# Performance work log

Hardware: AMD Instinct MI355X
Metric: run time of the kernel (lower is better)

Reference implementation:

```python
import jax, jax.numpy as jnp
import numpy as np
import math

B, S, H, D = 4, 4096, 2048, 128  # batch, seq_len, hidden_dim, head_size

def setup_inputs() -> dict:
    key = jax.random.key(0)
    ks = jax.random.split(key, 7)
    scale = 1.0 / math.sqrt(H)
    return {
        "x": jax.random.normal(ks[0], (B, S, H), dtype=jnp.float32),
        "Wq": jax.random.normal(ks[1], (H, D), dtype=jnp.float32) * scale,
        "bq": jnp.zeros((D,), dtype=jnp.float32),
        "Wk": jax.random.normal(ks[2], (H, D), dtype=jnp.float32) * scale,
        "bk": jnp.zeros((D,), dtype=jnp.float32),
        "Wv": jax.random.normal(ks[3], (H, D), dtype=jnp.float32) * scale,
        "bv": jnp.zeros((D,), dtype=jnp.float32),
    }

def reference(x, Wq, bq, Wk, bk, Wv, bv):
    # projections: [B,S,D]
    q = x @ Wq + bq
    k = x @ Wk + bk
    v = x @ Wv + bv
    # raw scores [B,S,S] with causal mask, NO pre-softmax scaling (as in source)
    scores = jnp.einsum('bsd,btd->bst', q, k)
    causal = jnp.tril(jnp.ones((S, S), dtype=bool))
    scores = jnp.where(causal, scores, -jnp.inf)
    # non-standard: scale AFTER softmax by 1/sqrt(head_size)
    w = jax.nn.softmax(scores, axis=-1) * (1.0 / math.sqrt(D))
    # dropout p=0.0 -> identity
    return jnp.einsum('bst,btd->bsd', w, v)
```

## Files before the change

kernel.cpp:

```cpp
#include <hip/hip_runtime.h>
#include <math.h>
#include <stdint.h>

#define SEQ   4096
#define HID   2048
#define HD    128
#define NROWS 16384

typedef __attribute__((ext_vector_type(8))) short bf16x8;
typedef __attribute__((ext_vector_type(4))) float f32x4;

static constexpr float OSCALE = 0.088388347648318447f;

using gvptr = const __attribute__((address_space(1))) void*;
using lvptr = __attribute__((address_space(3))) void*;
__device__ __forceinline__ void gld_lds16(const void* g, void* l) {
    __builtin_amdgcn_global_load_lds((gvptr)g, (lvptr)l, 16, 0, 0);
}

__device__ __forceinline__ unsigned short f2bf_rne(float f) {
    union { float f; unsigned u; } v; v.f = f;
    unsigned u = v.u + 0x7fffu + ((v.u >> 16) & 1u);
    return (unsigned short)(u >> 16);
}
__device__ __forceinline__ unsigned short f2bf_tr(float f) {
    union { float f; unsigned u; } v; v.f = f;
    return (unsigned short)(v.u >> 16);
}
__device__ __forceinline__ float bf2f(unsigned short h) {
    union { unsigned u; float f; } v; v.u = ((unsigned)h) << 16;
    return v.f;
}

__global__ __launch_bounds__(256) void prep_w(
    const float* __restrict__ Wq, const float* __restrict__ Wk, const float* __restrict__ Wv,
    unsigned short* __restrict__ wth, unsigned short* __restrict__ wtl)
{
    __shared__ float T[64][68];
    const int tid = threadIdx.x;
    const int k0 = blockIdx.x * 64, n0 = blockIdx.y * 64, mm = blockIdx.z;
    const float* W = (mm == 0) ? Wq : (mm == 1) ? Wk : Wv;
    #pragma unroll
    for (int i = 0; i < 4; ++i) {
        const int fi = i * 256 + tid, kk = fi >> 4, nc = (fi & 15) * 4;
        const float4 w = *(const float4*)(W + (size_t)(k0 + kk) * HD + n0 + nc);
        T[kk][nc] = w.x; T[kk][nc + 1] = w.y; T[kk][nc + 2] = w.z; T[kk][nc + 3] = w.w;
    }
    __syncthreads();
    unsigned short* oh = wth + (size_t)mm * HD * HID;
    unsigned short* ol = wtl + (size_t)mm * HD * HID;
    #pragma unroll
    for (int i = 0; i < 4; ++i) {
        const int fi = i * 256 + tid, nn = fi >> 4, kc = (fi & 15) * 4;
        const float a = T[kc][nn], b = T[kc + 1][nn], c = T[kc + 2][nn], d = T[kc + 3][nn];
        ushort4 hv, lv;
        hv.x = f2bf_rne(a); hv.y = f2bf_rne(b); hv.z = f2bf_rne(c); hv.w = f2bf_rne(d);
        lv.x = f2bf_rne(a - bf2f(hv.x)); lv.y = f2bf_rne(b - bf2f(hv.y));
        lv.z = f2bf_rne(c - bf2f(hv.z)); lv.w = f2bf_rne(d - bf2f(hv.w));
        *(ushort4*)(oh + (size_t)(n0 + nn) * HID + k0 + kc) = hv;
        *(ushort4*)(ol + (size_t)(n0 + nn) * HID + k0 + kc) = lv;
    }
}

__global__ __launch_bounds__(256, 3) void qkv_split(
    const float* __restrict__ x,
    const float* __restrict__ bq, const float* __restrict__ bk, const float* __restrict__ bv,
    const unsigned short* __restrict__ wth, const unsigned short* __restrict__ wtl,
    unsigned short* __restrict__ qh, unsigned short* __restrict__ ql,
    unsigned short* __restrict__ kh, unsigned short* __restrict__ kl,
    unsigned short* __restrict__ vth)
{
    __shared__ unsigned short Ah[64][64], Al[64][64];
    __shared__ unsigned short Bh[128][64], Bl[128][64];

    const int tid = threadIdx.x, wave = tid >> 6, lane = tid & 63;
    const int l15 = lane & 15, q4 = lane >> 4;
    const int wr = wave >> 1, wc = wave & 1;
    const int type = blockIdx.x % 3;
    const int tile = blockIdx.x / 3;
    const int r0 = tile * 64;
    const bool qk = (type < 2);

    const unsigned short* wh = wth + (size_t)type * HD * HID;
    const unsigned short* wl = wtl + (size_t)type * HD * HID;

    const int srow   = lane >> 3;
    const int schunk = ((lane & 7) ^ srow) * 8;

    f32x4 acc[2][4];
    #pragma unroll
    for (int mt = 0; mt < 2; ++mt)
        #pragma unroll
        for (int nt = 0; nt < 4; ++nt)
            acc[mt][nt] = (f32x4){0.f, 0.f, 0.f, 0.f};

    const float* xbase = x + (size_t)r0 * HID;

    float4 xv[4];
    #pragma unroll
    for (int i = 0; i < 4; ++i) {
        const int fi = i * 256 + tid, row = fi >> 4, kc = (fi & 15) * 4;
        xv[i] = *(const float4*)(xbase + (size_t)row * HID + kc);
    }

    for (int k0 = 0; k0 < HID; k0 += 64) {
        __syncthreads();

        {
            #pragma unroll
            for (int c = 0; c < 4; ++c) {
                const int row = wave * 32 + c * 8;
                gld_lds16(wh + (size_t)(row + srow) * HID + k0 + schunk, &Bh[row][0]);
            }
            if (qk) {
                #pragma unroll
                for (int c = 0; c < 4; ++c) {
                    const int row = wave * 32 + c * 8;
                    gld_lds16(wl + (size_t)(row + srow) * HID + k0 + schunk, &Bl[row][0]);
                }
            }
        }
        #pragma unroll
        for (int i = 0; i < 4; ++i) {
            const int fi = i * 256 + tid, row = fi >> 4, kc = (fi & 15) * 4;
            const int pk = ((kc >> 3) ^ (row & 7)) * 8 + (kc & 7);
            ushort4 hv;
            hv.x = f2bf_tr(xv[i].x); hv.y = f2bf_tr(xv[i].y);
            hv.z = f2bf_tr(xv[i].z); hv.w = f2bf_tr(xv[i].w);
            *(ushort4*)&Ah[row][pk] = hv;
            if (qk) {
                ushort4 lv;
                lv.x = f2bf_tr(xv[i].x - bf2f(hv.x)); lv.y = f2bf_tr(xv[i].y - bf2f(hv.y));
                lv.z = f2bf_tr(xv[i].z - bf2f(hv.z)); lv.w = f2bf_tr(xv[i].w - bf2f(hv.w));
                *(ushort4*)&Al[row][pk] = lv;
            }
        }
        __syncthreads();

        const int kn = (k0 + 64 < HID) ? (k0 + 64) : 0;
        #pragma unroll
        for (int i = 0; i < 4; ++i) {
            const int fi = i * 256 + tid, row = fi >> 4, kc = (fi & 15) * 4;
            xv[i] = *(const float4*)(xbase + (size_t)row * HID + kn + kc);
        }

        #pragma unroll
        for (int ks = 0; ks < 2; ++ks) {
            const int pc = ((ks * 4 + q4) ^ (l15 & 7)) * 8;
            bf16x8 ah[2], al[2];
            #pragma unroll
            for (int mt = 0; mt < 2; ++mt) {
                const int ar = wr * 32 + mt * 16 + l15;
                ah[mt] = *(const bf16x8*)&Ah[ar][pc];
                if (qk) al[mt] = *(const bf16x8*)&Al[ar][pc];
            }
            #pragma unroll
            for (int nt = 0; nt < 4; ++nt) {
                const int br = wc * 64 + nt * 16 + l15;
                const bf16x8 bh = *(const bf16x8*)&Bh[br][pc];
                #pragma unroll
                for (int mt = 0; mt < 2; ++mt)
                    acc[mt][nt] = __builtin_amdgcn_mfma_f32_16x16x32_bf16(ah[mt], bh, acc[mt][nt], 0, 0, 0);
                if (qk) {
                    const bf16x8 bl = *(const bf16x8*)&Bl[br][pc];
                    #pragma unroll
                    for (int mt = 0; mt < 2; ++mt) {
                        acc[mt][nt] = __builtin_amdgcn_mfma_f32_16x16x32_bf16(ah[mt], bl, acc[mt][nt], 0, 0, 0);
                        acc[mt][nt] = __builtin_amdgcn_mfma_f32_16x16x32_bf16(al[mt], bh, acc[mt][nt], 0, 0, 0);
                    }
                }
            }
        }
    }

    if (qk) {
        const float* bb = (type == 0) ? bq : bk;
        unsigned short* oh = (type == 0) ? qh : kh;
        unsigned short* ol = (type == 0) ? ql : kl;
        #pragma unroll
        for (int nt = 0; nt < 4; ++nt) {
            const int col = wc * 64 + nt * 16 + l15;
            const float bias = bb[col];
            #pragma unroll
            for (int mt = 0; mt < 2; ++mt) {
                const int Rb = r0 + wr * 32 + mt * 16 + q4 * 4;
                #pragma unroll
                for (int r = 0; r < 4; ++r) {
                    const float v = acc[mt][nt][r] + bias;
                    const unsigned short h = f2bf_rne(v);
                    oh[(size_t)(Rb + r) * HD + col] = h;
                    ol[(size_t)(Rb + r) * HD + col] = f2bf_rne(v - bf2f(h));
                }
            }
        }
    } else {
        #pragma unroll
        for (int nt = 0; nt < 4; ++nt) {
            const int col = wc * 64 + nt * 16 + l15;
            const float bias = bv[col];
            #pragma unroll
            for (int mt = 0; mt < 2; ++mt) {
                const int Rb = r0 + wr * 32 + mt * 16 + q4 * 4;
                const int bi = Rb >> 12, s0 = Rb & 4095;
                ushort4 pv;
                pv.x = f2bf_rne(acc[mt][nt][0] + bias);
                pv.y = f2bf_rne(acc[mt][nt][1] + bias);
                pv.z = f2bf_rne(acc[mt][nt][2] + bias);
                pv.w = f2bf_rne(acc[mt][nt][3] + bias);
                *(ushort4*)(vth + ((size_t)(bi * HD + col)) * SEQ + s0) = pv;
            }
        }
    }
}

__global__ __launch_bounds__(256, 2) void flash_mfma(
    const unsigned short* __restrict__ qh, const unsigned short* __restrict__ ql,
    const unsigned short* __restrict__ kh, const unsigned short* __restrict__ kl,
    const unsigned short* __restrict__ vth,
    unsigned short* __restrict__ oPb, float* __restrict__ mP, float* __restrict__ lP)
{
    __shared__ unsigned short Kh[64][128], Kl[64][128];
    __shared__ unsigned short Vt[128][64];
    __shared__ unsigned short Ps[4][16][72];

    const int tid = threadIdx.x, wave = tid >> 6, lane = tid & 63;
    const int l15 = lane & 15, q4 = lane >> 4;
    const int h = blockIdx.x & 3, pair = (blockIdx.x >> 2) & 31, b = blockIdx.x >> 7;

    const int krow_l = lane >> 4;
    const int vrow_l = lane >> 3;
    const int vsc = ((lane & 7) ^ (vrow_l & 7)) * 8;
    const int kkey7 = l15 & 7;
    const int vkey7 = l15 & 7;

    for (int side = 0; side < 2; ++side) {
        const int tt = side ? (63 - pair) : pair;
        const int n = tt + 1;
        const int j0 = (n * h) >> 2, j1 = (n * (h + 1)) >> 2;

        const int qrow = b * SEQ + tt * 64 + wave * 16 + l15;
        bf16x8 aqh[4], aql[4];
        #pragma unroll
        for (int ks = 0; ks < 4; ++ks) {
            aqh[ks] = *(const bf16x8*)(qh + (size_t)qrow * HD + ks * 32 + q4 * 8);
            aql[ks] = *(const bf16x8*)(ql + (size_t)qrow * HD + ks * 32 + q4 * 8);
        }
        f32x4 oa[8];
        #pragma unroll
        for (int d = 0; d < 8; ++d) oa[d] = (f32x4){0.f, 0.f, 0.f, 0.f};
        float m_r[4] = {-INFINITY, -INFINITY, -INFINITY, -INFINITY};
        float l_r[4] = {0.f, 0.f, 0.f, 0.f};

        for (int j = j0; j < j1; ++j) {
            __syncthreads();
            {
                const size_t kb = (size_t)b * SEQ + j * 64;
                #pragma unroll
                for (int c = 0; c < 4; ++c) {
                    const int rl = c * 4 + krow_l;
                    const int sc = (l15 ^ (rl & 7)) * 8;
                    const size_t gr = (kb + wave * 16 + rl) * HD + sc;
                    gld_lds16(kh + gr, &Kh[wave * 16 + c * 4][0]);
                    gld_lds16(kl + gr, &Kl[wave * 16 + c * 4][0]);
                }
                #pragma unroll
                for (int c = 0; c < 4; ++c)
                    gld_lds16(vth + ((size_t)(b * HD + wave * 32 + c * 8 + vrow_l)) * SEQ
                                  + j * 64 + vsc,
                              &Vt[wave * 32 + c * 8][0]);
            }
            __syncthreads();

            f32x4 s[4];
            #pragma unroll
            for (int nt = 0; nt < 4; ++nt) s[nt] = (f32x4){0.f, 0.f, 0.f, 0.f};
            #pragma unroll
            for (int ks = 0; ks < 4; ++ks) {
                const int pc = ((ks * 4 + q4) ^ kkey7) * 8;
                #pragma unroll
                for (int nt = 0; nt < 4; ++nt) {
                    const bf16x8 bh = *(const bf16x8*)&Kh[nt * 16 + l15][pc];
                    const bf16x8 bl = *(const bf16x8*)&Kl[nt * 16 + l15][pc];
                    s[nt] = __builtin_amdgcn_mfma_f32_16x16x32_bf16(aqh[ks], bh, s[nt], 0, 0, 0);
                    s[nt] = __builtin_amdgcn_mfma_f32_16x16x32_bf16(aql[ks], bh, s[nt], 0, 0, 0);
                    s[nt] = __builtin_amdgcn_mfma_f32_16x16x32_bf16(aqh[ks], bl, s[nt], 0, 0, 0);
                }
            }
            if (j == tt) {
                #pragma unroll
                for (int nt = 0; nt < 4; ++nt) {
                    const int cl = nt * 16 + l15;
                    #pragma unroll
                    for (int r = 0; r < 4; ++r) {
                        const int rl = wave * 16 + q4 * 4 + r;
                        if (cl > rl) s[nt][r] = -INFINITY;
                    }
                }
            }
            #pragma unroll
            for (int r = 0; r < 4; ++r) {
                float mt = fmaxf(fmaxf(s[0][r], s[1][r]), fmaxf(s[2][r], s[3][r]));
                mt = fmaxf(mt, __shfl_xor(mt, 1));
                mt = fmaxf(mt, __shfl_xor(mt, 2));
                mt = fmaxf(mt, __shfl_xor(mt, 4));
                mt = fmaxf(mt, __shfl_xor(mt, 8));
                const float mn = fmaxf(m_r[r], mt);
                const float al = __expf(m_r[r] - mn);
                m_r[r] = mn;
                const float p0 = __expf(s[0][r] - mn), p1 = __expf(s[1][r] - mn);
                const float p2 = __expf(s[2][r] - mn), p3 = __expf(s[3][r] - mn);
                Ps[wave][q4 * 4 + r][l15]      = f2bf_tr(p0);
                Ps[wave][q4 * 4 + r][16 + l15] = f2bf_tr(p1);
                Ps[wave][q4 * 4 + r][32 + l15] = f2bf_tr(p2);
                Ps[wave][q4 * 4 + r][48 + l15] = f2bf_tr(p3);
                float ps = p0 + p1 + p2 + p3;
                ps += __shfl_xor(ps, 1); ps += __shfl_xor(ps, 2);
                ps += __shfl_xor(ps, 4); ps += __shfl_xor(ps, 8);
                l_r[r] = l_r[r] * al + ps;
                #pragma unroll
                for (int d = 0; d < 8; ++d) oa[d][r] *= al;
            }
            const bf16x8 ap0 = *(const bf16x8*)&Ps[wave][l15][q4 * 8];
            const bf16x8 ap1 = *(const bf16x8*)&Ps[wave][l15][32 + q4 * 8];
            #pragma unroll
            for (int d = 0; d < 8; ++d) {
                const bf16x8 bv0 = *(const bf16x8*)&Vt[d * 16 + l15][(q4 ^ vkey7) * 8];
                const bf16x8 bv1 = *(const bf16x8*)&Vt[d * 16 + l15][((4 + q4) ^ vkey7) * 8];
                oa[d] = __builtin_amdgcn_mfma_f32_16x16x32_bf16(ap0, bv0, oa[d], 0, 0, 0);
                oa[d] = __builtin_amdgcn_mfma_f32_16x16x32_bf16(ap1, bv1, oa[d], 0, 0, 0);
            }
        }

        const int R0 = b * SEQ + tt * 64 + wave * 16 + q4 * 4;
        unsigned short* op = oPb + (size_t)h * NROWS * HD;
        #pragma unroll
        for (int d = 0; d < 8; ++d)
            #pragma unroll
            for (int r = 0; r < 4; ++r)
                op[(size_t)(R0 + r) * HD + d * 16 + l15] = f2bf_rne(oa[d][r]);
        if (l15 == 0) {
            #pragma unroll
            for (int r = 0; r < 4; ++r) {
                mP[h * NROWS + R0 + r] = m_r[r];
                lP[h * NROWS + R0 + r] = l_r[r];
            }
        }
    }
}

__global__ __launch_bounds__(256) void flash_merge(
    const unsigned short* __restrict__ oPb, const float* __restrict__ mP,
    const float* __restrict__ lP, float* __restrict__ out)
{
    const int idx = blockIdx.x * 256 + threadIdx.x;
    const int r = idx >> 5, c = (idx & 31) * 4;
    float m[4], l[4];
    #pragma unroll
    for (int i = 0; i < 4; ++i) { m[i] = mP[i * NROWS + r]; l[i] = lP[i * NROWS + r]; }
    float M = fmaxf(fmaxf(m[0], m[1]), fmaxf(m[2], m[3]));
    float a[4], lsum = 0.f;
    #pragma unroll
    for (int i = 0; i < 4; ++i) { a[i] = __expf(m[i] - M); lsum += l[i] * a[i]; }
    const float inv = OSCALE / lsum;
    float ox = 0.f, oy = 0.f, oz = 0.f, ow = 0.f;
    #pragma unroll
    for (int i = 0; i < 4; ++i) {
        const ushort4 ov = *(const ushort4*)(oPb + (size_t)i * NROWS * HD + (size_t)r * HD + c);
        ox += a[i] * bf2f(ov.x); oy += a[i] * bf2f(ov.y);
        oz += a[i] * bf2f(ov.z); ow += a[i] * bf2f(ov.w);
    }
    float4 o; o.x = ox * inv; o.y = oy * inv; o.z = oz * inv; o.w = ow * inv;
    *(float4*)(out + (size_t)r * HD + c) = o;
}

extern "C" void kernel_launch(void* const* d_in, const int* in_sizes, int n_in,
                              void* d_out, int out_size, void* d_ws, size_t ws_size,
                              hipStream_t stream)
{
    (void)in_sizes; (void)n_in; (void)out_size; (void)ws_size;
    const float* x  = (const float*)d_in[0];
    const float* Wq = (const float*)d_in[1];
    const float* bq = (const float*)d_in[2];
    const float* Wk = (const float*)d_in[3];
    const float* bk = (const float*)d_in[4];
    const float* Wv = (const float*)d_in[5];
    const float* bv = (const float*)d_in[6];
    float* out = (float*)d_out;

    char* w = (char*)d_ws;
    unsigned short* qh  = (unsigned short*)(w);
    unsigned short* ql  = (unsigned short*)(w + 4194304);
    unsigned short* kh  = (unsigned short*)(w + 8388608);
    unsigned short* kl  = (unsigned short*)(w + 12582912);
    unsigned short* vth = (unsigned short*)(w + 16777216);
    unsigned short* wth = (unsigned short*)(w + 20971520);
    unsigned short* wtl = (unsigned short*)(w + 22544384);
    unsigned short* oPb = (unsigned short*)(w + 24117248);
    float* mP = (float*)(w + 40894464);
    float* lP = (float*)(w + 41156608);

    prep_w<<<dim3(32, 2, 3), 256, 0, stream>>>(Wq, Wk, Wv, wth, wtl);
    qkv_split<<<768, 256, 0, stream>>>(x, bq, bk, bv, wth, wtl, qh, ql, kh, kl, vth);
    flash_mfma<<<512, 256, 0, stream>>>(qh, ql, kh, kl, vth, oPb, mP, lP);
    flash_merge<<<2048, 256, 0, stream>>>(oPb, mP, lP, out);
}
```

Measured before the change: 311.4 us.

## Transpose QK^T MFMA layout, add lazy max rescale and MFMA priority hints

Swaps the MFMA operands for the score tile so each lane holds one query row's scores across its register slots. Row max and sum reductions then need only two cross-lane shuffles instead of four per row. The P tile is written to LDS as packed 4-wide stores. A wave-wide lazy rescale skips the exp correction and output rescale whenever no row's max grows by more than 8, and s_setprio is raised around the MFMA blocks. The lazy threshold lets unnormalized exponentials reach e^8, which is safe in fp32 but adds a per-tile vote and a branch.

Result: faster. 304.0 us (-2.4%).

```diff
diff --git a/kernel.cpp b/kernel.cpp
--- a/kernel.cpp
+++ b/kernel.cpp
@@ -248,8 +248,8 @@
         f32x4 oa[8];
         #pragma unroll
         for (int d = 0; d < 8; ++d) oa[d] = (f32x4){0.f, 0.f, 0.f, 0.f};
-        float m_r[4] = {-INFINITY, -INFINITY, -INFINITY, -INFINITY};
-        float l_r[4] = {0.f, 0.f, 0.f, 0.f};
+        float m_r = -INFINITY;
+        float l_r = 0.f;
 
         for (int j = j0; j < j1; ++j) {
             __syncthreads();
@@ -274,6 +274,7 @@
             f32x4 s[4];
             #pragma unroll
             for (int nt = 0; nt < 4; ++nt) s[nt] = (f32x4){0.f, 0.f, 0.f, 0.f};
+            __builtin_amdgcn_s_setprio(1);
             #pragma unroll
             for (int ks = 0; ks < 4; ++ks) {
                 const int pc = ((ks * 4 + q4) ^ kkey7) * 8;
@@ -281,47 +282,73 @@
                 for (int nt = 0; nt < 4; ++nt) {
                     const bf16x8 bh = *(const bf16x8*)&Kh[nt * 16 + l15][pc];
                     const bf16x8 bl = *(const bf16x8*)&Kl[nt * 16 + l15][pc];
-                    s[nt] = __builtin_amdgcn_mfma_f32_16x16x32_bf16(aqh[ks], bh, s[nt], 0, 0, 0);
-                    s[nt] = __builtin_amdgcn_mfma_f32_16x16x32_bf16(aql[ks], bh, s[nt], 0, 0, 0);
-                    s[nt] = __builtin_amdgcn_mfma_f32_16x16x32_bf16(aqh[ks], bl, s[nt], 0, 0, 0);
-                }
-            }
+                    s[nt] = __builtin_amdgcn_mfma_f32_16x16x32_bf16(bh, aqh[ks], s[nt], 0, 0, 0);
+                    s[nt] = __builtin_amdgcn_mfma_f32_16x16x32_bf16(bh, aql[ks], s[nt], 0, 0, 0);
+                    s[nt] = __builtin_amdgcn_mfma_f32_16x16x32_bf16(bl, aqh[ks], s[nt], 0, 0, 0);
+                }
+            }
+            __builtin_amdgcn_s_setprio(0);
+
             if (j == tt) {
-                #pragma unroll
-                for (int nt = 0; nt < 4; ++nt) {
-                    const int cl = nt * 16 + l15;
+                const int qloc = wave * 16 + l15;
+                #pragma unroll
+                for (int nt = 0; nt < 4; ++nt)
                     #pragma unroll
                     for (int r = 0; r < 4; ++r) {
-                        const int rl = wave * 16 + q4 * 4 + r;
-                        if (cl > rl) s[nt][r] = -INFINITY;
+                        const int kvl = nt * 16 + q4 * 4 + r;
+                        if (kvl > qloc) s[nt][r] = -INFINITY;
                     }
-                }
-            }
-            #pragma unroll
-            for (int r = 0; r < 4; ++r) {
-                float mt = fmaxf(fmaxf(s[0][r], s[1][r]), fmaxf(s[2][r], s[3][r]));
-                mt = fmaxf(mt, __shfl_xor(mt, 1));
-                mt = fmaxf(mt, __shfl_xor(mt, 2));
-                mt = fmaxf(mt, __shfl_xor(mt, 4));
-                mt = fmaxf(mt, __shfl_xor(mt, 8));
-                const float mn = fmaxf(m_r[r], mt);
-                const float al = __expf(m_r[r] - mn);
-                m_r[r] = mn;
-                const float p0 = __expf(s[0][r] - mn), p1 = __expf(s[1][r] - mn);
-                const float p2 = __expf(s[2][r] - mn), p3 = __expf(s[3][r] - mn);
-                Ps[wave][q4 * 4 + r][l15]      = f2bf_tr(p0);
-                Ps[wave][q4 * 4 + r][16 + l15] = f2bf_tr(p1);
-                Ps[wave][q4 * 4 + r][32 + l15] = f2bf_tr(p2);
-                Ps[wave][q4 * 4 + r][48 + l15] = f2bf_tr(p3);
-                float ps = p0 + p1 + p2 + p3;
-                ps += __shfl_xor(ps, 1); ps += __shfl_xor(ps, 2);
-                ps += __shfl_xor(ps, 4); ps += __shfl_xor(ps, 8);
-                l_r[r] = l_r[r] * al + ps;
-                #pragma unroll
-                for (int d = 0; d < 8; ++d) oa[d][r] *= al;
-            }
+            }
+
+            float mt = fmaxf(fmaxf(s[0][0], s[0][1]), fmaxf(s[0][2], s[0][3]));
+            #pragma unroll
+            for (int nt = 1; nt < 4; ++nt)
+                mt = fmaxf(mt, fmaxf(fmaxf(s[nt][0], s[nt][1]), fmaxf(s[nt][2], s[nt][3])));
+            mt = fmaxf(mt, __shfl_xor(mt, 16));
+            mt = fmaxf(mt, __shfl_xor(mt, 32));
+
+            const bool allskip = __all(mt <= m_r + 8.f);
+            const float mn = allskip ? m_r : fmaxf(m_r, mt);
+
+            f32x4 pf[4];
+            #pragma unroll
+            for (int nt = 0; nt < 4; ++nt)
+                #pragma unroll
+                for (int r = 0; r < 4; ++r)
+                    pf[nt][r] = __expf(s[nt][r] - mn);
+
+            #pragma unroll
+            for (int nt = 0; nt < 4; ++nt) {
+                ushort4 w;
+                w.x = f2bf_tr(pf[nt][0]); w.y = f2bf_tr(pf[nt][1]);
+                w.z = f2bf_tr(pf[nt][2]); w.w = f2bf_tr(pf[nt][3]);
+                *(ushort4*)&Ps[wave][l15][nt * 16 + q4 * 4] = w;
+            }
+
+            float ps = ((pf[0][0] + pf[0][1]) + (pf[0][2] + pf[0][3]))
+                     + ((pf[1][0] + pf[1][1]) + (pf[1][2] + pf[1][3]))
+                     + ((pf[2][0] + pf[2][1]) + (pf[2][2] + pf[2][3]))
+                     + ((pf[3][0] + pf[3][1]) + (pf[3][2] + pf[3][3]));
+            ps += __shfl_xor(ps, 16);
+            ps += __shfl_xor(ps, 32);
+
+            if (allskip) {
+                l_r += ps;
+            } else {
+                const float al = __expf(m_r - mn);
+                m_r = mn;
+                l_r = l_r * al + ps;
+                #pragma unroll
+                for (int r = 0; r < 4; ++r) {
+                    const float alr = __shfl(al, (q4 << 2) | r);
+                    #pragma unroll
+                    for (int d = 0; d < 8; ++d) oa[d][r] *= alr;
+                }
+            }
+
             const bf16x8 ap0 = *(const bf16x8*)&Ps[wave][l15][q4 * 8];
             const bf16x8 ap1 = *(const bf16x8*)&Ps[wave][l15][32 + q4 * 8];
+            __builtin_amdgcn_s_setprio(1);
             #pragma unroll
             for (int d = 0; d < 8; ++d) {
                 const bf16x8 bv0 = *(const bf16x8*)&Vt[d * 16 + l15][(q4 ^ vkey7) * 8];
@@ -329,6 +356,7 @@
                 oa[d] = __builtin_amdgcn_mfma_f32_16x16x32_bf16(ap0, bv0, oa[d], 0, 0, 0);
                 oa[d] = __builtin_amdgcn_mfma_f32_16x16x32_bf16(ap1, bv1, oa[d], 0, 0, 0);
             }
+            __builtin_amdgcn_s_setprio(0);
         }
 
         const int R0 = b * SEQ + tt * 64 + wave * 16 + q4 * 4;
@@ -338,12 +366,10 @@
             #pragma unroll
             for (int r = 0; r < 4; ++r)
                 op[(size_t)(R0 + r) * HD + d * 16 + l15] = f2bf_rne(oa[d][r]);
-        if (l15 == 0) {
-            #pragma unroll
-            for (int r = 0; r < 4; ++r) {
-                mP[h * NROWS + R0 + r] = m_r[r];
-                lP[h * NROWS + R0 + r] = l_r[r];
-            }
+        if (q4 == 0) {
+            const int qr = b * SEQ + tt * 64 + wave * 16 + l15;
+            mP[h * NROWS + qr] = m_r;
+            lP[h * NROWS + qr] = l_r;
         }
     }
 }
```
